# Optimization experiments

Hardware: AMD Instinct MI355X
Metric: run time of the kernel (lower is better)

Reference implementation:

```python
import jax, jax.numpy as jnp
import numpy as np

SIGMA = 1.0


def _rbf_gram(A, B):
    # A: (Tb, N, C), B: (Tb, M, C) -> (Tb, N, M)
    AA = jnp.sum(A * A, axis=2, keepdims=True)          # (Tb, N, 1)
    BB = jnp.sum(B * B, axis=2, keepdims=True)          # (Tb, M, 1)
    d = AA + jnp.swapaxes(BB, 1, 2) - 2.0 * jnp.einsum('bnc,bmc->bnm', A, B)
    return jnp.exp(-d / (2.0 * SIGMA ** 2))


def setup_inputs() -> dict:
    key = jax.random.key(0)
    kx, ky = jax.random.split(key)
    x = jax.random.normal(kx, (512, 128, 16), dtype=jnp.float32)
    y = jax.random.normal(ky, (512, 128, 16), dtype=jnp.float32)
    return {"x": x, "y": y}


def reference(x, y):
    # x, y: (batch, stream, channel)
    x_fds = jnp.concatenate((x[:, :-1, :], x[:, 1:, :]), axis=1)  # (B, 2(T-1), C)
    y_fds = jnp.concatenate((y[:, :-1, :], y[:, 1:, :]), axis=1)
    xf = jnp.transpose(x_fds, (1, 0, 2))  # (2(T-1), B, C)
    yf = jnp.transpose(y_fds, (1, 0, 2))

    N = xf.shape[1]
    Kxx = _rbf_gram(xf, xf)  # (2(T-1), N, N)
    # off-diagonal mean per batch: (sum - trace) / (N*(N-1))
    e_xx = (Kxx.sum(axis=(1, 2)) - jnp.trace(Kxx, axis1=1, axis2=2)) / (N * (N - 1))
    E_k_x1_x2 = e_xx.mean()

    Kxy = _rbf_gram(xf, yf)
    E_k_x_y = Kxy.mean(axis=(1, 2)).mean()

    return E_k_x1_x2 - 2.0 * E_k_x_y
```

## Files before the change

### kernel.cpp

```cpp
#include <hip/hip_runtime.h>


#define LOG2E 1.4426950408889634f
#define SCALE 1.2011224087864498f

#define XH_OFF   0u
#define XL_OFF   524288u
#define YH_OFF   1048576u
#define YL_OFF   1572864u
#define GX_OFF   2097152u
#define CSX_OFF  2162688u
#define CSY_OFF  2228224u
#define PART_OFF 2293760u

typedef __attribute__((ext_vector_type(8))) __bf16 bf16x8;
typedef __attribute__((ext_vector_type(4))) float floatx4;

union FragU { uint4 q; unsigned int u[4]; bf16x8 v; };

static __device__ __forceinline__ int off(int n) { return (n << 3) + ((n >> 2) << 2); }

static __device__ __forceinline__ unsigned short bfbits(__bf16 h) {
    union { __bf16 h; unsigned short s; } u; u.h = h; return u.s;
}
static __device__ __forceinline__ unsigned int packhh(__bf16 a, __bf16 b) {
    return (unsigned int)bfbits(a) | ((unsigned int)bfbits(b) << 16);
}

__global__ __launch_bounds__(256) void prep_kernel(const float* __restrict__ x,
                                                   const float* __restrict__ y,
                                                   unsigned int* __restrict__ ws) {
    const int bid = blockIdx.x, tid = threadIdx.x;
    const int m   = bid >> 8;
    const int t   = (bid >> 1) & 127;
    const int row = ((bid & 1) << 8) + tid;

    const float4* __restrict__ src4 = m ? (const float4*)y : (const float4*)x;
    const size_t gb = (size_t)row * 512 + t * 4;
    float4 f0 = src4[gb], f1 = src4[gb + 1], f2 = src4[gb + 2], f3 = src4[gb + 3];
    const float fs[16] = { f0.x, f0.y, f0.z, f0.w, f1.x, f1.y, f1.z, f1.w,
                           f2.x, f2.y, f2.z, f2.w, f3.x, f3.y, f3.z, f3.w };
    float g = 0.f;
    unsigned int hw[8], lw[8];
#pragma unroll
    for (int p = 0; p < 8; ++p) {
        const float v0 = fs[2 * p], v1 = fs[2 * p + 1];
        g += v0 * v0 + v1 * v1;
        const float s0 = v0 * SCALE, s1 = v1 * SCALE;
        const __bf16 h0 = (__bf16)s0, h1 = (__bf16)s1;
        hw[p] = packhh(h0, h1);
        lw[p] = packhh((__bf16)(s0 - (float)h0), (__bf16)(s1 - (float)h1));
    }
    const float gp = 0.5f * LOG2E * g;
    const unsigned int idx = (unsigned int)t * 512u + (unsigned int)row;
    unsigned int* __restrict__ H = ws + (m ? YH_OFF : XH_OFF) + (size_t)idx * 8;
    unsigned int* __restrict__ L = ws + (m ? YL_OFF : XL_OFF) + (size_t)idx * 8;
    *(uint4*)&H[0] = make_uint4(hw[0], hw[1], hw[2], hw[3]);
    *(uint4*)&H[4] = make_uint4(hw[4], hw[5], hw[6], hw[7]);
    *(uint4*)&L[0] = make_uint4(lw[0], lw[1], lw[2], lw[3]);
    *(uint4*)&L[4] = make_uint4(lw[4], lw[5], lw[6], lw[7]);
    float* __restrict__ wsf = (float*)ws;
    wsf[(m ? CSY_OFF : CSX_OFF) + idx] = __builtin_amdgcn_exp2f(-gp);
    if (!m) wsf[GX_OFF + idx] = gp;
}

__global__ __launch_bounds__(256, 4) void gram_kernel(const unsigned int* __restrict__ ws,
                                                      float* __restrict__ part) {
    __shared__ unsigned int BH[1152], BL[1152];
    __shared__ float csB[128], srg[128];
    __shared__ float red[4];

    const int slot = blockIdx.x;
    const int t    = blockIdx.y;
    const int tid  = threadIdx.x;
    const int w    = tid >> 6;
    const int lane = tid & 63;
    const int quad = lane >> 4;
    const int l15  = lane & 15;
    const int qh   = quad & 1;
    const float* __restrict__ wsf = (const float*)ws;

    int sa, sq, isxx;
    if (slot < 16) { isxx = 0; sa = slot >> 2; sq = slot & 3; }
    else {
        isxx = 1;
        const int s = slot - 16;
        if      (s < 4) { sa = 0; sq = s; }
        else if (s < 7) { sa = 1; sq = s - 3; }
        else if (s < 9) { sa = 2; sq = s - 5; }
        else            { sa = 3; sq = 3; }
    }

    {
        const int r = tid & 127;
        const unsigned int base = isxx ? ((tid < 128) ? XH_OFF : XL_OFF)
                                       : ((tid < 128) ? YH_OFF : YL_OFF);
        const unsigned int* __restrict__ g =
            ws + base + (unsigned int)((t * 512 + sq * 128 + r) << 3);
        uint4 q0 = *(const uint4*)&g[0];
        uint4 q1 = *(const uint4*)&g[4];
        unsigned int* __restrict__ dst = (tid < 128) ? BH : BL;
        *(uint4*)&dst[off(r)]     = q0;
        *(uint4*)&dst[off(r) + 4] = q1;
        if (tid < 128) csB[r] = wsf[(isxx ? CSX_OFF : CSY_OFF) + t * 512 + sq * 128 + r];
        else           srg[r] = wsf[GX_OFF + t * 512 + sa * 128 + r];
    }

    bf16x8 a1f[2], a2f[2];
    {
        FragU z; z.q = make_uint4(0u, 0u, 0u, 0u);
        const unsigned int hbase = (quad < 2) ? XH_OFF : XL_OFF;
#pragma unroll
        for (int rt = 0; rt < 2; ++rt) {
            const int row = sa * 128 + w * 32 + rt * 16 + l15;
            const unsigned int* __restrict__ p =
                ws + hbase + (unsigned int)((t * 512 + row) << 3) + qh * 4;
            FragU u; u.q = *(const uint4*)p;
            a1f[rt] = u.v;
            a2f[rt] = (quad < 2) ? u.v : z.v;
        }
    }
    __syncthreads();

    float sum[2][4] = {{0.f, 0.f, 0.f, 0.f}, {0.f, 0.f, 0.f, 0.f}};

    floatx4 accP[2], accC[2];
    float csP;
    {
        const int rb = off(l15) + qh * 4;
        FragU bh, bl;
        bh.q = *(const uint4*)&BH[rb];
        bl.q = *(const uint4*)&BL[rb];
        csP = csB[l15];
        floatx4 zc = {0.f, 0.f, 0.f, 0.f};
        accP[0] = __builtin_amdgcn_mfma_f32_16x16x32_bf16(a1f[0], bh.v, zc, 0, 0, 0);
        accP[0] = __builtin_amdgcn_mfma_f32_16x16x32_bf16(a2f[0], bl.v, accP[0], 0, 0, 0);
        accP[1] = __builtin_amdgcn_mfma_f32_16x16x32_bf16(a1f[1], bh.v, zc, 0, 0, 0);
        accP[1] = __builtin_amdgcn_mfma_f32_16x16x32_bf16(a2f[1], bl.v, accP[1], 0, 0, 0);
    }
#pragma unroll
    for (int jt = 1; jt < 8; ++jt) {
        const int n  = jt * 16 + l15;
        const int rb = off(n) + qh * 4;
        FragU bh, bl;
        bh.q = *(const uint4*)&BH[rb];
        bl.q = *(const uint4*)&BL[rb];
        const float cs = csB[n];
        floatx4 zc = {0.f, 0.f, 0.f, 0.f};
        accC[0] = __builtin_amdgcn_mfma_f32_16x16x32_bf16(a1f[0], bh.v, zc, 0, 0, 0);
        accC[0] = __builtin_amdgcn_mfma_f32_16x16x32_bf16(a2f[0], bl.v, accC[0], 0, 0, 0);
        accC[1] = __builtin_amdgcn_mfma_f32_16x16x32_bf16(a1f[1], bh.v, zc, 0, 0, 0);
        accC[1] = __builtin_amdgcn_mfma_f32_16x16x32_bf16(a2f[1], bl.v, accC[1], 0, 0, 0);
#pragma unroll
        for (int rt = 0; rt < 2; ++rt)
#pragma unroll
            for (int r = 0; r < 4; ++r)
                sum[rt][r] = fmaf(__builtin_amdgcn_exp2f(accP[rt][r]), csP, sum[rt][r]);
        accP[0] = accC[0];
        accP[1] = accC[1];
        csP = cs;
    }
#pragma unroll
    for (int rt = 0; rt < 2; ++rt)
#pragma unroll
        for (int r = 0; r < 4; ++r)
            sum[rt][r] = fmaf(__builtin_amdgcn_exp2f(accP[rt][r]), csP, sum[rt][r]);

    float tot = 0.f;
#pragma unroll
    for (int rt = 0; rt < 2; ++rt)
#pragma unroll
        for (int r = 0; r < 4; ++r) {
            const float rs = __builtin_amdgcn_exp2f(-srg[w * 32 + rt * 16 + quad * 4 + r]);
            tot = fmaf(sum[rt][r], rs, tot);
        }
    for (int o = 32; o > 0; o >>= 1) tot += __shfl_down(tot, o, 64);
    if (lane == 0) red[w] = tot;
    __syncthreads();
    if (tid == 0) {
        float wt = (t == 0 || t == 127) ? 1.f : 2.f;
        if (isxx && sq > sa) wt *= 2.f;
        const int idx = isxx ? (2048 + t * 10 + (slot - 16)) : (t * 16 + slot);
        part[idx] = wt * (red[0] + red[1] + red[2] + red[3]);
    }
}

__global__ __launch_bounds__(256) void finalize_kernel(const float* __restrict__ part,
                                                       float* __restrict__ out) {
    const int tid = threadIdx.x;
    double vxy = 0.0, vxx = 0.0;
#pragma unroll
    for (int k = 0; k < 8; ++k)  vxy += (double)part[tid + 256 * k];
#pragma unroll
    for (int k = 8; k < 13; ++k) vxx += (double)part[tid + 256 * k];
    for (int o = 32; o > 0; o >>= 1) {
        vxx += __shfl_down(vxx, o, 64);
        vxy += __shfl_down(vxy, o, 64);
    }
    __shared__ double red[8];
    const int wid = tid >> 6;
    if ((tid & 63) == 0) { red[wid] = vxx; red[4 + wid] = vxy; }
    __syncthreads();
    if (tid == 0) {
        double sxx = red[0] + red[1] + red[2] + red[3];
        double sxy = red[4] + red[5] + red[6] + red[7];
        double e1 = (sxx - 254.0 * 512.0) / (254.0 * 512.0 * 511.0);
        double e2 = sxy / (254.0 * 512.0 * 512.0);
        out[0] = (float)(e1 - 2.0 * e2);
    }
}

extern "C" void kernel_launch(void* const* d_in, const int* in_sizes, int n_in,
                              void* d_out, int out_size, void* d_ws, size_t ws_size,
                              hipStream_t stream) {
    (void)in_sizes; (void)n_in; (void)out_size; (void)ws_size;
    const float* x = (const float*)d_in[0];
    const float* y = (const float*)d_in[1];
    float* out = (float*)d_out;
    unsigned int* ws = (unsigned int*)d_ws;
    float* part = (float*)d_ws + PART_OFF;

    prep_kernel<<<dim3(512), dim3(256), 0, stream>>>(x, y, ws);
    gram_kernel<<<dim3(26, 128), dim3(256), 0, stream>>>(ws, part);
    finalize_kernel<<<dim3(1), dim3(256), 0, stream>>>(part, out);
}
```

Baseline: 79.68 us.

## Fuse prep, gram and finalize into one kernel with atomic reduction

Drops the separate prep and finalize kernels. Each gram block now loads its own fp32 rows from x/y, does the bf16 hi/lo split and the squared-norm terms in shared memory, and accumulates its partial sum into global double accumulators with atomics. The last block, found through an atomic counter, writes the final result. This removes two kernel launches and the workspace round-trip, but adds redundant prep work across blocks, strided fp32 global reads, atomic contention, and a memset launch.

```diff
diff --git a/kernel.cpp b/kernel.cpp
--- a/kernel.cpp
+++ b/kernel.cpp
@@ -3,15 +3,6 @@
 
 #define LOG2E 1.4426950408889634f
 #define SCALE 1.2011224087864498f
-
-#define XH_OFF   0u
-#define XL_OFF   524288u
-#define YH_OFF   1048576u
-#define YL_OFF   1572864u
-#define GX_OFF   2097152u
-#define CSX_OFF  2162688u
-#define CSY_OFF  2228224u
-#define PART_OFF 2293760u
 
 typedef __attribute__((ext_vector_type(8))) __bf16 bf16x8;
 typedef __attribute__((ext_vector_type(4))) float floatx4;
@@ -27,46 +18,15 @@
     return (unsigned int)bfbits(a) | ((unsigned int)bfbits(b) << 16);
 }
 
-__global__ __launch_bounds__(256) void prep_kernel(const float* __restrict__ x,
-                                                   const float* __restrict__ y,
-                                                   unsigned int* __restrict__ ws) {
-    const int bid = blockIdx.x, tid = threadIdx.x;
-    const int m   = bid >> 8;
-    const int t   = (bid >> 1) & 127;
-    const int row = ((bid & 1) << 8) + tid;
+#define NSLOT 26
+#define NBLK  (NSLOT * 128)
 
-    const float4* __restrict__ src4 = m ? (const float4*)y : (const float4*)x;
-    const size_t gb = (size_t)row * 512 + t * 4;
-    float4 f0 = src4[gb], f1 = src4[gb + 1], f2 = src4[gb + 2], f3 = src4[gb + 3];
-    const float fs[16] = { f0.x, f0.y, f0.z, f0.w, f1.x, f1.y, f1.z, f1.w,
-                           f2.x, f2.y, f2.z, f2.w, f3.x, f3.y, f3.z, f3.w };
-    float g = 0.f;
-    unsigned int hw[8], lw[8];
-#pragma unroll
-    for (int p = 0; p < 8; ++p) {
-        const float v0 = fs[2 * p], v1 = fs[2 * p + 1];
-        g += v0 * v0 + v1 * v1;
-        const float s0 = v0 * SCALE, s1 = v1 * SCALE;
-        const __bf16 h0 = (__bf16)s0, h1 = (__bf16)s1;
-        hw[p] = packhh(h0, h1);
-        lw[p] = packhh((__bf16)(s0 - (float)h0), (__bf16)(s1 - (float)h1));
-    }
-    const float gp = 0.5f * LOG2E * g;
-    const unsigned int idx = (unsigned int)t * 512u + (unsigned int)row;
-    unsigned int* __restrict__ H = ws + (m ? YH_OFF : XH_OFF) + (size_t)idx * 8;
-    unsigned int* __restrict__ L = ws + (m ? YL_OFF : XL_OFF) + (size_t)idx * 8;
-    *(uint4*)&H[0] = make_uint4(hw[0], hw[1], hw[2], hw[3]);
-    *(uint4*)&H[4] = make_uint4(hw[4], hw[5], hw[6], hw[7]);
-    *(uint4*)&L[0] = make_uint4(lw[0], lw[1], lw[2], lw[3]);
-    *(uint4*)&L[4] = make_uint4(lw[4], lw[5], lw[6], lw[7]);
-    float* __restrict__ wsf = (float*)ws;
-    wsf[(m ? CSY_OFF : CSX_OFF) + idx] = __builtin_amdgcn_exp2f(-gp);
-    if (!m) wsf[GX_OFF + idx] = gp;
-}
-
-__global__ __launch_bounds__(256, 4) void gram_kernel(const unsigned int* __restrict__ ws,
-                                                      float* __restrict__ part) {
-    __shared__ unsigned int BH[1152], BL[1152];
+__global__ __launch_bounds__(256, 4) void mmd_kernel(const float* __restrict__ x,
+                                                     const float* __restrict__ y,
+                                                     double* __restrict__ acc,
+                                                     unsigned int* __restrict__ cnt,
+                                                     float* __restrict__ out) {
+    __shared__ unsigned int AH[1152], AL[1152], BH[1152], BL[1152];
     __shared__ float csB[128], srg[128];
     __shared__ float red[4];
 
@@ -78,7 +38,6 @@
     const int quad = lane >> 4;
     const int l15  = lane & 15;
     const int qh   = quad & 1;
-    const float* __restrict__ wsf = (const float*)ws;
 
     int sa, sq, isxx;
     if (slot < 16) { isxx = 0; sa = slot >> 2; sq = slot & 3; }
@@ -92,35 +51,52 @@
     }
 
     {
-        const int r = tid & 127;
-        const unsigned int base = isxx ? ((tid < 128) ? XH_OFF : XL_OFF)
-                                       : ((tid < 128) ? YH_OFF : YL_OFF);
-        const unsigned int* __restrict__ g =
-            ws + base + (unsigned int)((t * 512 + sq * 128 + r) << 3);
-        uint4 q0 = *(const uint4*)&g[0];
-        uint4 q1 = *(const uint4*)&g[4];
-        unsigned int* __restrict__ dst = (tid < 128) ? BH : BL;
-        *(uint4*)&dst[off(r)]     = q0;
-        *(uint4*)&dst[off(r) + 4] = q1;
-        if (tid < 128) csB[r] = wsf[(isxx ? CSX_OFF : CSY_OFF) + t * 512 + sq * 128 + r];
-        else           srg[r] = wsf[GX_OFF + t * 512 + sa * 128 + r];
+        const int half = tid >> 7;
+        const int r    = tid & 127;
+        const int grow = (half ? sq : sa) * 128 + r;
+        const float4* __restrict__ src4 =
+            (half && !isxx) ? (const float4*)y : (const float4*)x;
+        const size_t gb = (size_t)grow * 512 + t * 4;
+        float4 f0 = src4[gb], f1 = src4[gb + 1], f2 = src4[gb + 2], f3 = src4[gb + 3];
+        const float fs[16] = { f0.x, f0.y, f0.z, f0.w, f1.x, f1.y, f1.z, f1.w,
+                               f2.x, f2.y, f2.z, f2.w, f3.x, f3.y, f3.z, f3.w };
+        float g = 0.f;
+        unsigned int hw[8], lw[8];
+#pragma unroll
+        for (int p = 0; p < 8; ++p) {
+            const float v0 = fs[2 * p], v1 = fs[2 * p + 1];
+            g += v0 * v0 + v1 * v1;
+            const float s0 = v0 * SCALE, s1 = v1 * SCALE;
+            const __bf16 h0 = (__bf16)s0, h1 = (__bf16)s1;
+            hw[p] = packhh(h0, h1);
+            lw[p] = packhh((__bf16)(s0 - (float)h0), (__bf16)(s1 - (float)h1));
+        }
+        const float gp = 0.5f * LOG2E * g;
+        unsigned int* __restrict__ H = half ? BH : AH;
+        unsigned int* __restrict__ L = half ? BL : AL;
+        const int o = off(r);
+        *(uint4*)&H[o]     = make_uint4(hw[0], hw[1], hw[2], hw[3]);
+        *(uint4*)&H[o + 4] = make_uint4(hw[4], hw[5], hw[6], hw[7]);
+        *(uint4*)&L[o]     = make_uint4(lw[0], lw[1], lw[2], lw[3]);
+        *(uint4*)&L[o + 4] = make_uint4(lw[4], lw[5], lw[6], lw[7]);
+        if (half) csB[r] = __builtin_amdgcn_exp2f(-gp);
+        else      srg[r] = gp;
     }
+    __syncthreads();
 
     bf16x8 a1f[2], a2f[2];
     {
         FragU z; z.q = make_uint4(0u, 0u, 0u, 0u);
-        const unsigned int hbase = (quad < 2) ? XH_OFF : XL_OFF;
 #pragma unroll
         for (int rt = 0; rt < 2; ++rt) {
-            const int row = sa * 128 + w * 32 + rt * 16 + l15;
-            const unsigned int* __restrict__ p =
-                ws + hbase + (unsigned int)((t * 512 + row) << 3) + qh * 4;
-            FragU u; u.q = *(const uint4*)p;
+            const int row = w * 32 + rt * 16 + l15;
+            const int rb  = off(row) + qh * 4;
+            FragU u;
+            u.q = (quad < 2) ? *(const uint4*)&AH[rb] : *(const uint4*)&AL[rb];
             a1f[rt] = u.v;
             a2f[rt] = (quad < 2) ? u.v : z.v;
         }
     }
-    __syncthreads();
 
     float sum[2][4] = {{0.f, 0.f, 0.f, 0.f}, {0.f, 0.f, 0.f, 0.f}};
 
@@ -180,33 +156,19 @@
     if (tid == 0) {
         float wt = (t == 0 || t == 127) ? 1.f : 2.f;
         if (isxx && sq > sa) wt *= 2.f;
-        const int idx = isxx ? (2048 + t * 10 + (slot - 16)) : (t * 16 + slot);
-        part[idx] = wt * (red[0] + red[1] + red[2] + red[3]);
-    }
-}
-
-__global__ __launch_bounds__(256) void finalize_kernel(const float* __restrict__ part,
-                                                       float* __restrict__ out) {
-    const int tid = threadIdx.x;
-    double vxy = 0.0, vxx = 0.0;
-#pragma unroll
-    for (int k = 0; k < 8; ++k)  vxy += (double)part[tid + 256 * k];
-#pragma unroll
-    for (int k = 8; k < 13; ++k) vxx += (double)part[tid + 256 * k];
-    for (int o = 32; o > 0; o >>= 1) {
-        vxx += __shfl_down(vxx, o, 64);
-        vxy += __shfl_down(vxy, o, 64);
-    }
-    __shared__ double red[8];
-    const int wid = tid >> 6;
-    if ((tid & 63) == 0) { red[wid] = vxx; red[4 + wid] = vxy; }
-    __syncthreads();
-    if (tid == 0) {
-        double sxx = red[0] + red[1] + red[2] + red[3];
-        double sxy = red[4] + red[5] + red[6] + red[7];
-        double e1 = (sxx - 254.0 * 512.0) / (254.0 * 512.0 * 511.0);
-        double e2 = sxy / (254.0 * 512.0 * 512.0);
-        out[0] = (float)(e1 - 2.0 * e2);
+        const double part = (double)(wt * (red[0] + red[1] + red[2] + red[3]));
+        atomicAdd(&acc[isxx], part);
+        __threadfence();
+        const unsigned int old = atomicAdd(cnt, 1u);
+        if (old == NBLK - 1) {
+            const double sxy = __hip_atomic_load(&acc[0], __ATOMIC_RELAXED,
+                                                 __HIP_MEMORY_SCOPE_AGENT);
+            const double sxx = __hip_atomic_load(&acc[1], __ATOMIC_RELAXED,
+                                                 __HIP_MEMORY_SCOPE_AGENT);
+            const double e1 = (sxx - 254.0 * 512.0) / (254.0 * 512.0 * 511.0);
+            const double e2 = sxy / (254.0 * 512.0 * 512.0);
+            out[0] = (float)(e1 - 2.0 * e2);
+        }
     }
 }
 
@@ -217,10 +179,9 @@
     const float* x = (const float*)d_in[0];
     const float* y = (const float*)d_in[1];
     float* out = (float*)d_out;
-    unsigned int* ws = (unsigned int*)d_ws;
-    float* part = (float*)d_ws + PART_OFF;
+    double* acc = (double*)d_ws;
+    unsigned int* cnt = (unsigned int*)((char*)d_ws + 16);
 
-    prep_kernel<<<dim3(512), dim3(256), 0, stream>>>(x, y, ws);
-    gram_kernel<<<dim3(26, 128), dim3(256), 0, stream>>>(ws, part);
-    finalize_kernel<<<dim3(1), dim3(256), 0, stream>>>(part, out);
+    hipMemsetAsync(d_ws, 0, 64, stream);
+    mmd_kernel<<<dim3(NSLOT, 128), dim3(256), 0, stream>>>(x, y, acc, cnt, out);
 }
```

Result: slower. 152.1 us (+90.9%).
